# Kernel optimization log

Hardware: AMD Instinct MI355X
Metric: run time of the kernel (lower is better)

Reference implementation:

```python
import jax, jax.numpy as jnp
import numpy as np

B, T, C, NH, L, V = 2, 1024, 768, 12, 4, 50304
HS = C // NH  # 64


def _norm(x):
    # torch: (x - x.mean(-1)) / x.std(-1) with unbiased std (ddof=1)
    mu = jnp.mean(x, axis=-1, keepdims=True)
    sd = jnp.std(x, axis=-1, ddof=1, keepdims=True)
    return (x - mu) / sd


def setup_inputs() -> dict:
    key = jax.random.key(0)
    ks = jax.random.split(key, 8)
    idx = jax.random.randint(ks[0], (B, T), 0, V)
    wte = jax.random.normal(ks[1], (V, C), jnp.float32) * 0.02
    wpe = jax.random.normal(ks[2], (1024, C), jnp.float32) * 0.02
    c_attn_w = jax.random.normal(ks[3], (L, 3 * C, C), jnp.float32) * 0.02
    c_proj_w = jax.random.normal(ks[4], (L, C, C), jnp.float32) * 0.02
    w_decay = jax.random.uniform(ks[5], (L, C), jnp.float32)          # decay in [0,1)
    eta = jax.random.uniform(ks[6], (L, C), jnp.float32) * 0.01       # small, like 1/block_size init
    lm_head_w = jax.random.normal(ks[7], (V, C), jnp.float32) * 0.02
    return dict(idx=idx, wte=wte, wpe=wpe, c_attn_w=c_attn_w, c_proj_w=c_proj_w,
                w_decay=w_decay, eta=eta, lm_head_w=lm_head_w)


def _rwkv7_block(x, Wqkv, Wproj, wd, et):
    Bx, Tx, Cx = x.shape
    qkv = (x @ Wqkv.T).reshape(Bx, Tx, 3, NH, HS)
    qkv = _norm(qkv)
    # [T, B, nh, hs] each
    q = jnp.transpose(qkv[:, :, 0], (1, 0, 2, 3))
    k = jnp.transpose(qkv[:, :, 1], (1, 0, 2, 3))
    v = jnp.transpose(qkv[:, :, 2], (1, 0, 2, 3))
    q = jax.lax.erf(q)
    k = jax.lax.erf(k)
    wv = wd.reshape(NH, HS)   # decay per (head, channel i)
    ev = et.reshape(NH, HS)
    a = -k
    b = k * ev
    k_ = k * ev
    v_ = v

    def step(state, inp):
        q_t, a_t, b_t, k_t, v_t = inp
        # state: [B, nh, hs(i), hs(k)]
        sab = jnp.einsum('bhik,bhk,bhj->bhij', state, a_t, b_t)
        state = state * wv[None, :, :, None] + sab + jnp.einsum('bhj,bhi->bhij', k_t, v_t)
        out = jnp.einsum('bhj,bhij->bhi', q_t, state)
        return state, out

    state0 = jnp.zeros((Bx, NH, HS, HS), x.dtype)
    _, vt = jax.lax.scan(step, state0, (q, a, b, k_, v_))  # vt: [T, B, nh, hs]
    y = jnp.transpose(vt, (1, 0, 2, 3)).reshape(Bx, Tx, Cx) @ Wproj.T
    return x + y


def reference(idx, wte, wpe, c_attn_w, c_proj_w, w_decay, eta, lm_head_w):
    t = idx.shape[1]
    x = wte[idx] + wpe[:t][None]
    for l in range(L):
        x = _rwkv7_block(x, c_attn_w[l], c_proj_w[l], w_decay[l], eta[l])
    x = _norm(x)
    # targets=None path: logits for last position only
    logits = x[:, -1:, :] @ lm_head_w.T  # [B, 1, V]
    return logits
```

## Files before the change

kernel.cpp:

```cpp
#include <hip/hip_runtime.h>
#include <hip/hip_bf16.h>
#include <cmath>

using bf16   = __bf16;
using bf16x8 = __attribute__((ext_vector_type(8))) __bf16;
using bf16x4 = __attribute__((ext_vector_type(4))) __bf16;
using f32x4  = __attribute__((ext_vector_type(4))) float;
using u32x4  = __attribute__((ext_vector_type(4))) unsigned int;

__global__ __launch_bounds__(256) void cast4_kernel(const float* __restrict__ src,
                                                    bf16* __restrict__ dst, int n4) {
  int i = blockIdx.x * 256 + threadIdx.x;
  int stride = gridDim.x * 256;
  for (; i < n4; i += stride) {
    f32x4 v = ((const f32x4*)src)[i];
    bf16x4 o;
    o[0] = (bf16)v[0]; o[1] = (bf16)v[1]; o[2] = (bf16)v[2]; o[3] = (bf16)v[3];
    ((bf16x4*)dst)[i] = o;
  }
}

__global__ __launch_bounds__(256) void emb_kernel(const int* __restrict__ idx,
                                                  const float* __restrict__ wte,
                                                  const float* __restrict__ wpe,
                                                  float* __restrict__ xf,
                                                  bf16* __restrict__ xb) {
  int bt = blockIdx.x;
  int t = bt & 1023;
  int tok = idx[bt];
  const float* wr = wte + (long)tok * 768;
  const float* pr = wpe + (long)t * 768;
  for (int c = threadIdx.x; c < 768; c += 256) {
    float v = wr[c] + pr[c];
    xf[(long)bt * 768 + c] = v;
    xb[(long)bt * 768 + c] = (bf16)v;
  }
}

template <int PROJ>
__global__ __launch_bounds__(256) void gemm_kernel(const bf16* __restrict__ A,
                                                   const bf16* __restrict__ W,
                                                   float* __restrict__ out,
                                                   float* __restrict__ xf,
                                                   bf16* __restrict__ xb,
                                                   int N, int K) {
  __shared__ char ldsA[128 * 128];
  __shared__ char ldsB[128 * 128];
  const int tid = threadIdx.x;
  const int l = tid & 63, wid = tid >> 6;
  const int lr = l & 15, g = l >> 4;
  const int m0 = blockIdx.y * 128, n0 = blockIdx.x * 128;
  const int wm = wid >> 1, wn = wid & 1;

  f32x4 acc[4][4];
#pragma unroll
  for (int i = 0; i < 4; ++i)
#pragma unroll
    for (int j = 0; j < 4; ++j) acc[i][j] = {0.f, 0.f, 0.f, 0.f};

  for (int k0 = 0; k0 < K; k0 += 32) {
    __syncthreads();
#pragma unroll
    for (int it = 0; it < 2; ++it) {
      int slot = tid + it * 256;
      int row = slot >> 2, q = slot & 3;
      u32x4 da = *(const u32x4*)(A + (long)(m0 + row) * K + k0 + q * 8);
      *(u32x4*)(ldsA + row * 128 + ((q * 16) ^ ((row & 7) << 4))) = da;
      u32x4 db = *(const u32x4*)(W + (long)(n0 + row) * K + k0 + q * 8);
      *(u32x4*)(ldsB + row * 128 + ((q * 16) ^ ((row & 7) << 4))) = db;
    }
    __syncthreads();
    bf16x8 af[4], bfr[4];
#pragma unroll
    for (int it = 0; it < 4; ++it) {
      int row = wm * 64 + it * 16 + lr;
      af[it] = *(const bf16x8*)(ldsA + row * 128 + ((16 * g) ^ ((row & 7) << 4)));
    }
#pragma unroll
    for (int jt = 0; jt < 4; ++jt) {
      int row = wn * 64 + jt * 16 + lr;
      bfr[jt] = *(const bf16x8*)(ldsB + row * 128 + ((16 * g) ^ ((row & 7) << 4)));
    }
#pragma unroll
    for (int it = 0; it < 4; ++it)
#pragma unroll
      for (int jt = 0; jt < 4; ++jt)
        acc[it][jt] = __builtin_amdgcn_mfma_f32_16x16x32_bf16(af[it], bfr[jt], acc[it][jt], 0, 0, 0);
  }

#pragma unroll
  for (int it = 0; it < 4; ++it) {
#pragma unroll
    for (int jt = 0; jt < 4; ++jt) {
      int col = n0 + wn * 64 + jt * 16 + lr;
#pragma unroll
      for (int r = 0; r < 4; ++r) {
        int row = m0 + wm * 64 + it * 16 + g * 4 + r;
        if constexpr (PROJ) {
          long o = (long)row * 768 + col;
          float v = acc[it][jt][r] + xf[o];
          xf[o] = v;
          xb[o] = (bf16)v;
        } else {
          out[(long)row * N + col] = acc[it][jt][r];
        }
      }
    }
  }
}

__global__ __launch_bounds__(256) void normerf_kernel(const float* __restrict__ qkv,
                                                      const float* __restrict__ eta_l,
                                                      bf16* __restrict__ qG,
                                                      bf16* __restrict__ aG,
                                                      bf16* __restrict__ bG,
                                                      float* __restrict__ vG) {
  int gidx = blockIdx.x * 4 + (threadIdx.x >> 6);
  int lane = threadIdx.x & 63;
  int h = gidx % 12;
  int rest = gidx / 12;
  int s = rest % 3;
  int bt = rest / 3;
  float x = qkv[(long)bt * 2304 + s * 768 + h * 64 + lane];
  float mu = x;
#pragma unroll
  for (int o = 32; o; o >>= 1) mu += __shfl_xor(mu, o);
  mu *= (1.f / 64.f);
  float d = x - mu;
  float v2 = d * d;
#pragma unroll
  for (int o = 32; o; o >>= 1) v2 += __shfl_xor(v2, o);
  float sd = sqrtf(v2 * (1.f / 63.f));
  float gn = d / sd;
  int b = bt >> 10, t = bt & 1023;
  long base = ((long)(b * 12 + h) * 1024 + t) * 64 + lane;
  if (s == 0) {
    qG[base] = (bf16)erff(gn);
  } else if (s == 1) {
    float kh = erff(gn);
    aG[base] = (bf16)(-kh);
    bG[base] = (bf16)(kh * eta_l[h * 64 + lane]);
  } else {
    vG[base] = gn;
  }
}

__global__ __launch_bounds__(256) void gram_kernel(const bf16* __restrict__ aG,
                                                   const bf16* __restrict__ bG,
                                                   const bf16* __restrict__ qG,
                                                   float* __restrict__ GaG,
                                                   bf16* __restrict__ GqG,
                                                   bf16* __restrict__ bTG) {
  const int bh = blockIdx.x >> 6, ch = blockIdx.x & 63;
  __shared__ float as[16][68], bs[16][68], qs[16][68];
  const long tb = ((long)bh * 1024 + ch * 16) * 64;
  for (int i = threadIdx.x; i < 1024; i += 256) {
    int t = i >> 6, d = i & 63;
    as[t][d] = (float)aG[tb + i];
    bs[t][d] = (float)bG[tb + i];
    qs[t][d] = (float)qG[tb + i];
  }
  __syncthreads();
  const int t = threadIdx.x & 15, u = threadIdx.x >> 4;
  float dba = 0.f, dbq = 0.f;
#pragma unroll 4
  for (int d = 0; d < 64; ++d) {
    float bv = bs[u][d];
    dba += bv * as[t][d];
    dbq += bv * qs[t][d];
  }
  long g2 = (long)bh * 64 + ch;
  GaG[g2 * 256 + u * 16 + t] = (u < t) ? dba : 0.f;
  GqG[g2 * 512 + t * 32 + u] = (u <= t) ? (bf16)dbq : (bf16)0.f;
  GqG[g2 * 512 + t * 32 + 16 + u] = (bf16)0.f;
  int j = threadIdx.x >> 2, uq = threadIdx.x & 3;
  bf16x8 pkv;
#pragma unroll
  for (int uu = 0; uu < 8; ++uu) pkv[uu] = (uq < 2) ? (bf16)bs[uq * 8 + uu][j] : (bf16)0.f;
  *(bf16x8*)(bTG + g2 * 2048 + j * 32 + uq * 8) = pkv;
}

__global__ __launch_bounds__(256) void scan_kernel(const float* __restrict__ wdl,
                                                   const bf16* __restrict__ aG,
                                                   const bf16* __restrict__ qG,
                                                   const float* __restrict__ vG,
                                                   const float* __restrict__ GaG,
                                                   const bf16* __restrict__ GqG,
                                                   const bf16* __restrict__ bTG,
                                                   bf16* __restrict__ yG) {
  const int bh = blockIdx.x;
  const int b = bh / 12, h = bh - b * 12;
  const int tid = threadIdx.x;
  const int l = tid & 63, wid = tid >> 6;
  const int lr = l & 15, g = l >> 4;

  __shared__ char sA[2][16 * 128];
  __shared__ char sQ[2][16 * 128];
  __shared__ char sB[2][64 * 128];
  __shared__ char sG[2][16 * 128];
  __shared__ float sGa[2][16][16];
  __shared__ float sV[2][16][68];
  __shared__ char sS[64 * 128];
  __shared__ float sM[16][68];

  const float* wrow = wdl + h * 64;
  const int irow = wid * 16 + lr;
  const float w_rec = fmaxf(wrow[irow], 0.004f);
  const float winv_rec = 1.0f / w_rec;

  float wc[4], w15c[4], l2wc[4];
#pragma unroll
  for (int r = 0; r < 4; ++r) {
    int row = wid * 16 + g * 4 + r;
    float w = fmaxf(wrow[row], 0.004f);
    wc[r] = w;
    l2wc[r] = log2f(w);
    w15c[r] = exp2f(15.0f * l2wc[r]);
  }

  f32x4 Sf[4];
#pragma unroll
  for (int j = 0; j < 4; ++j) Sf[j] = {0.f, 0.f, 0.f, 0.f};

  const long hTD = (long)bh * 1024 * 64;

  u32x4 rAQ, rB, rGG;
  f32x4 rV;

  auto LOAD = [&](int c) {
    const long tb = hTD + (long)c * 16 * 64;
    const long g2 = (long)bh * 64 + c;
    if (tid < 128) {
      rAQ = *(const u32x4*)(aG + tb + (tid >> 3) * 64 + (tid & 7) * 8);
    } else {
      rAQ = *(const u32x4*)(qG + tb + ((tid - 128) >> 3) * 64 + ((tid - 128) & 7) * 8);
    }
    rB = *(const u32x4*)(bTG + g2 * 2048 + (tid >> 2) * 32 + (tid & 3) * 8);
    if (tid < 64) {
      rGG = *(const u32x4*)(GqG + g2 * 512 + (tid >> 2) * 32 + (tid & 3) * 8);
    } else if (tid < 128) {
      rGG = *(const u32x4*)(GaG + g2 * 256 + ((tid - 64) >> 2) * 16 + ((tid - 64) & 3) * 4);
    }
    rV = *(const f32x4*)(vG + tb + (tid >> 4) * 64 + (tid & 15) * 4);
  };

  auto STORE = [&](int nb) {
    if (tid < 128) {
      int t = tid >> 3, q = tid & 7;
      *(u32x4*)(sA[nb] + t * 128 + ((q * 16) ^ ((t & 7) << 4))) = rAQ;
    } else {
      int t = (tid - 128) >> 3, q = (tid - 128) & 7;
      *(u32x4*)(sQ[nb] + t * 128 + ((q * 16) ^ ((t & 7) << 4))) = rAQ;
    }
    {
      int j = tid >> 2, q = tid & 3;
      *(u32x4*)(sB[nb] + j * 128 + ((q * 16) ^ ((j & 7) << 4))) = rB;
    }
    if (tid < 64) {
      int t = tid >> 2, q = tid & 3;
      *(u32x4*)(sG[nb] + t * 128 + ((q * 16) ^ ((t & 7) << 4))) = rGG;
    } else if (tid < 128) {
      int u = (tid - 64) >> 2, q = (tid - 64) & 3;
      *(u32x4*)(&sGa[nb][u][q * 4]) = rGG;
    }
    {
      int t = tid >> 4, i4 = tid & 15;
      *(f32x4*)(&sV[nb][t][i4 * 4]) = rV;
    }
  };

  LOAD(0);
  STORE(0);
#pragma unroll
  for (int jt = 0; jt < 4; ++jt) {
#pragma unroll
    for (int r = 0; r < 4; ++r) {
      int row = wid * 16 + g * 4 + r;
      int d = jt * 16 + lr;
      *(bf16*)(sS + row * 128 + ((d * 2) ^ ((row & 7) << 4))) = (bf16)0.0f;
    }
  }
  __syncthreads();

  for (int ch = 0; ch < 64; ++ch) {
    const int cur = ch & 1, nxt = cur ^ 1;
    if (ch < 63) LOAD(ch + 1);

    f32x4 mf = {0.f, 0.f, 0.f, 0.f}, mqf = {0.f, 0.f, 0.f, 0.f};
#pragma unroll
    for (int s = 0; s < 2; ++s) {
      bf16x8 af = *(const bf16x8*)(sS + irow * 128 + ((64 * s + 16 * g) ^ ((irow & 7) << 4)));
      bf16x8 ba = *(const bf16x8*)(sA[cur] + lr * 128 + ((64 * s + 16 * g) ^ ((lr & 7) << 4)));
      bf16x8 bq = *(const bf16x8*)(sQ[cur] + lr * 128 + ((64 * s + 16 * g) ^ ((lr & 7) << 4)));
      mf = __builtin_amdgcn_mfma_f32_16x16x32_bf16(af, ba, mf, 0, 0, 0);
      mqf = __builtin_amdgcn_mfma_f32_16x16x32_bf16(af, bq, mqf, 0, 0, 0);
    }
#pragma unroll
    for (int r = 0; r < 4; ++r) sM[lr][wid * 16 + g * 4 + r] = mf[r];
    asm volatile("s_waitcnt lgkmcnt(0)" ::: "memory");
    __builtin_amdgcn_sched_barrier(0);

    float accr[16];
#pragma unroll
    for (int t = 0; t < 16; ++t) accr[t] = 0.f;
    bf16x8 zfrag;
#pragma unroll
    for (int i = 0; i < 8; ++i) zfrag[i] = (bf16)0.0f;
    float wp = 1.f, wpm1 = 0.f, wiv = 1.f;
#pragma unroll
    for (int u = 0; u < 16; ++u) {
      float mu = sM[u][irow];
      float vu = sV[cur][u][irow];
      float c = wp * mu + wpm1 * accr[u];
      float zt = wiv * (c + vu);
      zfrag[u & 7] = (g == (u >> 3)) ? (bf16)zt : zfrag[u & 7];
      f32x4 ga0 = *(const f32x4*)(&sGa[cur][u][0]);
      f32x4 ga1 = *(const f32x4*)(&sGa[cur][u][4]);
      f32x4 ga2 = *(const f32x4*)(&sGa[cur][u][8]);
      f32x4 ga3 = *(const f32x4*)(&sGa[cur][u][12]);
#pragma unroll
      for (int t = 0; t < 4; ++t) {
        accr[t] += ga0[t] * zt;
        accr[4 + t] += ga1[t] * zt;
        accr[8 + t] += ga2[t] * zt;
        accr[12 + t] += ga3[t] * zt;
      }
      wpm1 = wp;
      wp *= w_rec;
      wiv *= winv_rec;
    }

    {
      bf16x8 gq = *(const bf16x8*)(sG[cur] + lr * 128 + ((16 * g) ^ ((lr & 7) << 4)));
      f32x4 cy;
#pragma unroll
      for (int r = 0; r < 4; ++r) cy[r] = mqf[r] * wc[r];
      f32x4 yp = __builtin_amdgcn_mfma_f32_16x16x32_bf16(zfrag, gq, cy, 0, 0, 0);
      int t = lr;
      bf16x4 yo;
#pragma unroll
      for (int r = 0; r < 4; ++r) yo[r] = (bf16)(yp[r] * exp2f((float)t * l2wc[r]));
      long yoff = ((long)b * 1024 + ch * 16 + t) * 768 + h * 64 + wid * 16 + g * 4;
      *(bf16x4*)(yG + yoff) = yo;
    }

#pragma unroll
    for (int jt = 0; jt < 4; ++jt) {
      int jrow = jt * 16 + lr;
      bf16x8 bb = *(const bf16x8*)(sB[cur] + jrow * 128 + ((16 * g) ^ ((jrow & 7) << 4)));
      f32x4 cs;
#pragma unroll
      for (int r = 0; r < 4; ++r) cs[r] = Sf[jt][r] * wc[r];
      f32x4 ns = __builtin_amdgcn_mfma_f32_16x16x32_bf16(zfrag, bb, cs, 0, 0, 0);
#pragma unroll
      for (int r = 0; r < 4; ++r) Sf[jt][r] = ns[r] * w15c[r];
    }

#pragma unroll
    for (int jt = 0; jt < 4; ++jt) {
#pragma unroll
      for (int r = 0; r < 4; ++r) {
        int row = wid * 16 + g * 4 + r;
        int d = jt * 16 + lr;
        *(bf16*)(sS + row * 128 + ((d * 2) ^ ((row & 7) << 4))) = (bf16)Sf[jt][r];
      }
    }

    if (ch < 63) STORE(nxt);
    __syncthreads();
  }
}

__global__ __launch_bounds__(256) void finalnorm_kernel(const float* __restrict__ xf,
                                                        float* __restrict__ xn) {
  __shared__ float red[4];
  int tid = threadIdx.x;
  for (int b = 0; b < 2; ++b) {
    const float* xr = xf + ((long)b * 1024 + 1023) * 768;
    float s = 0.f;
    for (int c = tid; c < 768; c += 256) s += xr[c];
#pragma unroll
    for (int o = 32; o; o >>= 1) s += __shfl_xor(s, o);
    if ((tid & 63) == 0) red[tid >> 6] = s;
    __syncthreads();
    float mu = (red[0] + red[1] + red[2] + red[3]) * (1.f / 768.f);
    __syncthreads();
    float s2 = 0.f;
    for (int c = tid; c < 768; c += 256) {
      float d = xr[c] - mu;
      s2 += d * d;
    }
#pragma unroll
    for (int o = 32; o; o >>= 1) s2 += __shfl_xor(s2, o);
    if ((tid & 63) == 0) red[tid >> 6] = s2;
    __syncthreads();
    float sd = sqrtf((red[0] + red[1] + red[2] + red[3]) * (1.f / 767.f));
    for (int c = tid; c < 768; c += 256) xn[b * 768 + c] = (xr[c] - mu) / sd;
    __syncthreads();
  }
}

__global__ __launch_bounds__(256) void lmhead_kernel(const float* __restrict__ W,
                                                     const float* __restrict__ xn,
                                                     float* __restrict__ out) {
  int l = threadIdx.x & 63, wid = threadIdx.x >> 6;
  int v0 = blockIdx.x * 64 + wid * 16;
  f32x4 x0[3], x1[3];
#pragma unroll
  for (int i = 0; i < 3; ++i) {
    x0[i] = *(const f32x4*)(xn + l * 4 + i * 256);
    x1[i] = *(const f32x4*)(xn + 768 + l * 4 + i * 256);
  }
  for (int vi = 0; vi < 16; ++vi) {
    const float* wr = W + (long)(v0 + vi) * 768;
    float pa = 0.f, pb = 0.f;
#pragma unroll
    for (int i = 0; i < 3; ++i) {
      f32x4 wv = *(const f32x4*)(wr + l * 4 + i * 256);
#pragma unroll
      for (int r = 0; r < 4; ++r) {
        pa += wv[r] * x0[i][r];
        pb += wv[r] * x1[i][r];
      }
    }
#pragma unroll
    for (int o = 32; o; o >>= 1) {
      pa += __shfl_xor(pa, o);
      pb += __shfl_xor(pb, o);
    }
    if (l == 0) {
      out[v0 + vi] = pa;
      out[50304 + v0 + vi] = pb;
    }
  }
}

extern "C" void kernel_launch(void* const* d_in, const int* in_sizes, int n_in,
                              void* d_out, int out_size, void* d_ws, size_t ws_size,
                              hipStream_t stream) {
  (void)in_sizes; (void)n_in; (void)out_size; (void)ws_size;
  const int*   idx      = (const int*)d_in[0];
  const float* wte      = (const float*)d_in[1];
  const float* wpe      = (const float*)d_in[2];
  const float* c_attn_w = (const float*)d_in[3];
  const float* c_proj_w = (const float*)d_in[4];
  const float* w_decay  = (const float*)d_in[5];
  const float* eta      = (const float*)d_in[6];
  const float* lm_head  = (const float*)d_in[7];
  float* out = (float*)d_out;

  char* ws = (char*)d_ws;
  size_t off = 0;
  auto alloc = [&](size_t bytes) -> char* {
    char* p = ws + off;
    off = (off + bytes + 255) & ~(size_t)255;
    return p;
  };
  float* xf   = (float*)alloc(2L * 1024 * 768 * 4);
  bf16*  xb   = (bf16*)alloc(2L * 1024 * 768 * 2);
  float* qkv  = (float*)alloc(2L * 1024 * 2304 * 4);
  bf16*  qGp  = (bf16*)alloc(24L * 1024 * 64 * 2);
  bf16*  aGp  = (bf16*)alloc(24L * 1024 * 64 * 2);
  bf16*  bGp  = (bf16*)alloc(24L * 1024 * 64 * 2);
  float* vGp  = (float*)alloc(24L * 1024 * 64 * 4);
  float* GaGp = (float*)alloc(24L * 64 * 256 * 4);
  bf16*  GqGp = (bf16*)alloc(24L * 64 * 512 * 2);
  bf16*  bTGp = (bf16*)alloc(24L * 64 * 2048 * 2);
  bf16*  yGp  = (bf16*)alloc(2L * 1024 * 768 * 2);
  bf16*  WqB  = (bf16*)alloc(4L * 2304 * 768 * 2);
  bf16*  WpB  = (bf16*)alloc(4L * 768 * 768 * 2);
  float* xn   = (float*)alloc(2L * 768 * 4);

  cast4_kernel<<<dim3(2048), dim3(256), 0, stream>>>(c_attn_w, WqB, 4 * 2304 * 768 / 4);
  cast4_kernel<<<dim3(1024), dim3(256), 0, stream>>>(c_proj_w, WpB, 4 * 768 * 768 / 4);
  emb_kernel<<<dim3(2048), dim3(256), 0, stream>>>(idx, wte, wpe, xf, xb);

  for (int l = 0; l < 4; ++l) {
    gemm_kernel<0><<<dim3(18, 16), dim3(256), 0, stream>>>(
        xb, WqB + (long)l * 2304 * 768, qkv, nullptr, nullptr, 2304, 768);
    normerf_kernel<<<dim3(18432), dim3(256), 0, stream>>>(
        qkv, eta + l * 768, qGp, aGp, bGp, vGp);
    gram_kernel<<<dim3(1536), dim3(256), 0, stream>>>(aGp, bGp, qGp, GaGp, GqGp, bTGp);
    scan_kernel<<<dim3(24), dim3(256), 0, stream>>>(
        w_decay + l * 768, aGp, qGp, vGp, GaGp, GqGp, bTGp, yGp);
    gemm_kernel<1><<<dim3(6, 16), dim3(256), 0, stream>>>(
        yGp, WpB + (long)l * 768 * 768, nullptr, xf, xb, 768, 768);
  }

  finalnorm_kernel<<<dim3(1), dim3(256), 0, stream>>>(xf, xn);
  lmhead_kernel<<<dim3(786), dim3(256), 0, stream>>>(lm_head, xn, out);
}
```

Before: 822.0 us.

## Fuse norm/erf into gram kernel and double-chunk scan prefetch

Merges the per-head normalization/erf kernel into the chunk gram kernel, so each block loads its raw qkv tile once and builds the gram products from shared memory without a global round trip for the b tensor. The scan kernel now prefetches two chunks per pipeline stage, which halves the number of block-wide barriers. It also tightens the shared-memory layout of the B and Gq tiles to 64-byte rows and gathers the per-chunk work into a COMPUTE lambda. The cost is more registers and shared memory in the scan, which runs only 24 blocks and is latency bound.

Result: faster. 797.9 us (-2.9%).

```diff
diff --git a/kernel.cpp b/kernel.cpp
--- a/kernel.cpp
+++ b/kernel.cpp
@@ -109,59 +109,65 @@
   }
 }
 
-__global__ __launch_bounds__(256) void normerf_kernel(const float* __restrict__ qkv,
-                                                      const float* __restrict__ eta_l,
-                                                      bf16* __restrict__ qG,
-                                                      bf16* __restrict__ aG,
-                                                      bf16* __restrict__ bG,
-                                                      float* __restrict__ vG) {
-  int gidx = blockIdx.x * 4 + (threadIdx.x >> 6);
-  int lane = threadIdx.x & 63;
-  int h = gidx % 12;
-  int rest = gidx / 12;
-  int s = rest % 3;
-  int bt = rest / 3;
-  float x = qkv[(long)bt * 2304 + s * 768 + h * 64 + lane];
-  float mu = x;
-#pragma unroll
-  for (int o = 32; o; o >>= 1) mu += __shfl_xor(mu, o);
-  mu *= (1.f / 64.f);
-  float d = x - mu;
-  float v2 = d * d;
-#pragma unroll
-  for (int o = 32; o; o >>= 1) v2 += __shfl_xor(v2, o);
-  float sd = sqrtf(v2 * (1.f / 63.f));
-  float gn = d / sd;
-  int b = bt >> 10, t = bt & 1023;
-  long base = ((long)(b * 12 + h) * 1024 + t) * 64 + lane;
-  if (s == 0) {
-    qG[base] = (bf16)erff(gn);
-  } else if (s == 1) {
-    float kh = erff(gn);
-    aG[base] = (bf16)(-kh);
-    bG[base] = (bf16)(kh * eta_l[h * 64 + lane]);
-  } else {
-    vG[base] = gn;
-  }
-}
-
-__global__ __launch_bounds__(256) void gram_kernel(const bf16* __restrict__ aG,
-                                                   const bf16* __restrict__ bG,
-                                                   const bf16* __restrict__ qG,
-                                                   float* __restrict__ GaG,
-                                                   bf16* __restrict__ GqG,
-                                                   bf16* __restrict__ bTG) {
+__global__ __launch_bounds__(256) void normgram_kernel(const float* __restrict__ qkv,
+                                                       const float* __restrict__ eta_l,
+                                                       bf16* __restrict__ qG,
+                                                       bf16* __restrict__ aG,
+                                                       float* __restrict__ vG,
+                                                       float* __restrict__ GaG,
+                                                       bf16* __restrict__ GqG,
+                                                       bf16* __restrict__ bTG) {
   const int bh = blockIdx.x >> 6, ch = blockIdx.x & 63;
+  const int b = bh / 12, h = bh - b * 12;
+  const int tid = threadIdx.x;
+  __shared__ float raw[48][68];
   __shared__ float as[16][68], bs[16][68], qs[16][68];
-  const long tb = ((long)bh * 1024 + ch * 16) * 64;
-  for (int i = threadIdx.x; i < 1024; i += 256) {
-    int t = i >> 6, d = i & 63;
-    as[t][d] = (float)aG[tb + i];
-    bs[t][d] = (float)bG[tb + i];
-    qs[t][d] = (float)qG[tb + i];
+
+  const long qbase = ((long)(b * 1024 + ch * 16)) * 2304 + h * 64;
+#pragma unroll
+  for (int i = 0; i < 3; ++i) {
+    int slot = tid + i * 256;
+    int c4 = slot & 15, sgrp = slot >> 4;
+    int t = sgrp / 3, s = sgrp - 3 * t;
+    f32x4 d = *(const f32x4*)(qkv + qbase + (long)t * 2304 + s * 768 + c4 * 4);
+    *(f32x4*)(&raw[sgrp][c4 * 4]) = d;
   }
   __syncthreads();
-  const int t = threadIdx.x & 15, u = threadIdx.x >> 4;
+
+  const int l = tid & 63, w = tid >> 6;
+  const float ev = eta_l[h * 64 + l];
+#pragma unroll
+  for (int j = 0; j < 12; ++j) {
+    int sgrp = w * 12 + j;
+    int t = sgrp / 3, s = sgrp - 3 * t;
+    float x = raw[sgrp][l];
+    float mu = x;
+#pragma unroll
+    for (int o = 32; o; o >>= 1) mu += __shfl_xor(mu, o);
+    mu *= (1.f / 64.f);
+    float d = x - mu;
+    float v2 = d * d;
+#pragma unroll
+    for (int o = 32; o; o >>= 1) v2 += __shfl_xor(v2, o);
+    float sd = sqrtf(v2 * (1.f / 63.f));
+    float gn = d / sd;
+    long base = ((long)bh * 1024 + ch * 16 + t) * 64 + l;
+    if (s == 0) {
+      float qv = erff(gn);
+      qs[t][l] = qv;
+      qG[base] = (bf16)qv;
+    } else if (s == 1) {
+      float kh = erff(gn);
+      as[t][l] = -kh;
+      bs[t][l] = kh * ev;
+      aG[base] = (bf16)(-kh);
+    } else {
+      vG[base] = gn;
+    }
+  }
+  __syncthreads();
+
+  const int t = tid & 15, u = tid >> 4;
   float dba = 0.f, dbq = 0.f;
 #pragma unroll 4
   for (int d = 0; d < 64; ++d) {
@@ -173,11 +179,11 @@
   GaG[g2 * 256 + u * 16 + t] = (u < t) ? dba : 0.f;
   GqG[g2 * 512 + t * 32 + u] = (u <= t) ? (bf16)dbq : (bf16)0.f;
   GqG[g2 * 512 + t * 32 + 16 + u] = (bf16)0.f;
-  int j = threadIdx.x >> 2, uq = threadIdx.x & 3;
+  int jj = tid >> 2, uq = tid & 3;
   bf16x8 pkv;
 #pragma unroll
-  for (int uu = 0; uu < 8; ++uu) pkv[uu] = (uq < 2) ? (bf16)bs[uq * 8 + uu][j] : (bf16)0.f;
-  *(bf16x8*)(bTG + g2 * 2048 + j * 32 + uq * 8) = pkv;
+  for (int uu = 0; uu < 8; ++uu) pkv[uu] = (uq < 2) ? (bf16)bs[uq * 8 + uu][jj] : (bf16)0.f;
+  *(bf16x8*)(bTG + g2 * 2048 + jj * 32 + uq * 8) = pkv;
 }
 
 __global__ __launch_bounds__(256) void scan_kernel(const float* __restrict__ wdl,
@@ -194,12 +200,12 @@
   const int l = tid & 63, wid = tid >> 6;
   const int lr = l & 15, g = l >> 4;
 
-  __shared__ char sA[2][16 * 128];
-  __shared__ char sQ[2][16 * 128];
-  __shared__ char sB[2][64 * 128];
-  __shared__ char sG[2][16 * 128];
-  __shared__ float sGa[2][16][16];
-  __shared__ float sV[2][16][68];
+  __shared__ char sA[2][2][16 * 128];
+  __shared__ char sQ[2][2][16 * 128];
+  __shared__ char sB[2][2][64 * 64];
+  __shared__ char sG[2][2][16 * 64];
+  __shared__ float sGa[2][2][16][16];
+  __shared__ float sV[2][2][16][64];
   __shared__ char sS[64 * 128];
   __shared__ float sM[16][68];
 
@@ -224,53 +230,147 @@
 
   const long hTD = (long)bh * 1024 * 64;
 
-  u32x4 rAQ, rB, rGG;
-  f32x4 rV;
-
-  auto LOAD = [&](int c) {
-    const long tb = hTD + (long)c * 16 * 64;
-    const long g2 = (long)bh * 64 + c;
-    if (tid < 128) {
-      rAQ = *(const u32x4*)(aG + tb + (tid >> 3) * 64 + (tid & 7) * 8);
-    } else {
-      rAQ = *(const u32x4*)(qG + tb + ((tid - 128) >> 3) * 64 + ((tid - 128) & 7) * 8);
-    }
-    rB = *(const u32x4*)(bTG + g2 * 2048 + (tid >> 2) * 32 + (tid & 3) * 8);
-    if (tid < 64) {
-      rGG = *(const u32x4*)(GqG + g2 * 512 + (tid >> 2) * 32 + (tid & 3) * 8);
-    } else if (tid < 128) {
-      rGG = *(const u32x4*)(GaG + g2 * 256 + ((tid - 64) >> 2) * 16 + ((tid - 64) & 3) * 4);
-    }
-    rV = *(const f32x4*)(vG + tb + (tid >> 4) * 64 + (tid & 15) * 4);
+  u32x4 rAQ[2], rB[2], rGG[2];
+  f32x4 rV[2];
+
+  auto LOAD2 = [&](int c0) {
+#pragma unroll
+    for (int k = 0; k < 2; ++k) {
+      const int c = c0 + k;
+      const long tb = hTD + (long)c * 16 * 64;
+      const long g2 = (long)bh * 64 + c;
+      if (tid < 128) {
+        rAQ[k] = *(const u32x4*)(aG + tb + (tid >> 3) * 64 + (tid & 7) * 8);
+      } else {
+        rAQ[k] = *(const u32x4*)(qG + tb + ((tid - 128) >> 3) * 64 + ((tid - 128) & 7) * 8);
+      }
+      rB[k] = *(const u32x4*)(bTG + g2 * 2048 + (tid >> 2) * 32 + (tid & 3) * 8);
+      if (tid < 64) {
+        rGG[k] = *(const u32x4*)(GqG + g2 * 512 + (tid >> 2) * 32 + (tid & 3) * 8);
+      } else if (tid < 128) {
+        rGG[k] = *(const u32x4*)(GaG + g2 * 256 + ((tid - 64) >> 2) * 16 + ((tid - 64) & 3) * 4);
+      }
+      rV[k] = *(const f32x4*)(vG + tb + (tid >> 4) * 64 + (tid & 15) * 4);
+    }
   };
 
-  auto STORE = [&](int nb) {
-    if (tid < 128) {
-      int t = tid >> 3, q = tid & 7;
-      *(u32x4*)(sA[nb] + t * 128 + ((q * 16) ^ ((t & 7) << 4))) = rAQ;
-    } else {
-      int t = (tid - 128) >> 3, q = (tid - 128) & 7;
-      *(u32x4*)(sQ[nb] + t * 128 + ((q * 16) ^ ((t & 7) << 4))) = rAQ;
-    }
+  auto STORE2 = [&](int nb) {
+#pragma unroll
+    for (int k = 0; k < 2; ++k) {
+      if (tid < 128) {
+        int t = tid >> 3, q = tid & 7;
+        *(u32x4*)(sA[nb][k] + t * 128 + ((q * 16) ^ ((t & 7) << 4))) = rAQ[k];
+      } else {
+        int t = (tid - 128) >> 3, q = (tid - 128) & 7;
+        *(u32x4*)(sQ[nb][k] + t * 128 + ((q * 16) ^ ((t & 7) << 4))) = rAQ[k];
+      }
+      {
+        int j = tid >> 2, q = tid & 3;
+        *(u32x4*)(sB[nb][k] + j * 64 + ((q * 16) ^ ((j & 3) << 4))) = rB[k];
+      }
+      if (tid < 64) {
+        int t = tid >> 2, q = tid & 3;
+        *(u32x4*)(sG[nb][k] + t * 64 + ((q * 16) ^ ((t & 3) << 4))) = rGG[k];
+      } else if (tid < 128) {
+        int u = (tid - 64) >> 2, q = (tid - 64) & 3;
+        *(u32x4*)(&sGa[nb][k][u][q * 4]) = rGG[k];
+      }
+      {
+        int t = tid >> 4, i4 = tid & 15;
+        *(f32x4*)(&sV[nb][k][t][i4 * 4]) = rV[k];
+      }
+    }
+  };
+
+  auto COMPUTE = [&](int cur, int cip, int ch) {
+    const char* pA = sA[cur][cip];
+    const char* pQ = sQ[cur][cip];
+    const char* pB = sB[cur][cip];
+    const char* pG = sG[cur][cip];
+    const float* pGa = &sGa[cur][cip][0][0];
+    const float* pV = &sV[cur][cip][0][0] + irow;
+    const float* pM = &sM[0][0] + irow;
+
+    asm volatile("s_waitcnt lgkmcnt(0)" ::: "memory");
+    __builtin_amdgcn_sched_barrier(0);
+
+    f32x4 mf = {0.f, 0.f, 0.f, 0.f}, mqf = {0.f, 0.f, 0.f, 0.f};
+#pragma unroll
+    for (int s = 0; s < 2; ++s) {
+      bf16x8 af = *(const bf16x8*)(sS + irow * 128 + ((64 * s + 16 * g) ^ ((irow & 7) << 4)));
+      bf16x8 ba = *(const bf16x8*)(pA + lr * 128 + ((64 * s + 16 * g) ^ ((lr & 7) << 4)));
+      bf16x8 bq = *(const bf16x8*)(pQ + lr * 128 + ((64 * s + 16 * g) ^ ((lr & 7) << 4)));
+      mf = __builtin_amdgcn_mfma_f32_16x16x32_bf16(af, ba, mf, 0, 0, 0);
+      mqf = __builtin_amdgcn_mfma_f32_16x16x32_bf16(af, bq, mqf, 0, 0, 0);
+    }
+#pragma unroll
+    for (int r = 0; r < 4; ++r) sM[lr][wid * 16 + g * 4 + r] = mf[r];
+    asm volatile("s_waitcnt lgkmcnt(0)" ::: "memory");
+    __builtin_amdgcn_sched_barrier(0);
+
+    f32x4 acc4[4];
+#pragma unroll
+    for (int t = 0; t < 4; ++t) acc4[t] = {0.f, 0.f, 0.f, 0.f};
+    bf16x8 zfrag;
+#pragma unroll
+    for (int i = 0; i < 8; ++i) zfrag[i] = (bf16)0.0f;
+    float wp = 1.f, wpm1 = 0.f, wiv = 1.f;
+#pragma unroll
+    for (int u = 0; u < 16; ++u) {
+      float muv = pM[u * 68];
+      float vu = pV[u * 64];
+      float c = wp * muv + wpm1 * acc4[u >> 2][u & 3];
+      float zt = wiv * (c + vu);
+      zfrag[u & 7] = (g == (u >> 3)) ? (bf16)zt : zfrag[u & 7];
+      f32x4 ztv = {zt, zt, zt, zt};
+#pragma unroll
+      for (int q = 0; q < 4; ++q) {
+        f32x4 ga = *(const f32x4*)(pGa + u * 16 + q * 4);
+        acc4[q] = __builtin_elementwise_fma(ga, ztv, acc4[q]);
+      }
+      wpm1 = wp;
+      wp *= w_rec;
+      wiv *= winv_rec;
+    }
+
+#pragma unroll
+    for (int jt = 0; jt < 4; ++jt) {
+      int jrow = jt * 16 + lr;
+      bf16x8 bb = *(const bf16x8*)(pB + jrow * 64 + ((16 * g) ^ ((jrow & 3) << 4)));
+      f32x4 cs;
+#pragma unroll
+      for (int r = 0; r < 4; ++r) cs[r] = Sf[jt][r] * wc[r];
+      f32x4 ns = __builtin_amdgcn_mfma_f32_16x16x32_bf16(zfrag, bb, cs, 0, 0, 0);
+#pragma unroll
+      for (int r = 0; r < 4; ++r) Sf[jt][r] = ns[r] * w15c[r];
+    }
+
+#pragma unroll
+    for (int jt = 0; jt < 4; ++jt) {
+#pragma unroll
+      for (int r = 0; r < 4; ++r) {
+        int row = wid * 16 + g * 4 + r;
+        int d = jt * 16 + lr;
+        *(bf16*)(sS + row * 128 + ((d * 2) ^ ((row & 7) << 4))) = (bf16)Sf[jt][r];
+      }
+    }
+
     {
-      int j = tid >> 2, q = tid & 3;
-      *(u32x4*)(sB[nb] + j * 128 + ((q * 16) ^ ((j & 7) << 4))) = rB;
-    }
-    if (tid < 64) {
-      int t = tid >> 2, q = tid & 3;
-      *(u32x4*)(sG[nb] + t * 128 + ((q * 16) ^ ((t & 7) << 4))) = rGG;
-    } else if (tid < 128) {
-      int u = (tid - 64) >> 2, q = (tid - 64) & 3;
-      *(u32x4*)(&sGa[nb][u][q * 4]) = rGG;
-    }
-    {
-      int t = tid >> 4, i4 = tid & 15;
-      *(f32x4*)(&sV[nb][t][i4 * 4]) = rV;
+      bf16x8 gq = *(const bf16x8*)(pG + lr * 64 + ((16 * g) ^ ((lr & 3) << 4)));
+      f32x4 cy;
+#pragma unroll
+      for (int r = 0; r < 4; ++r) cy[r] = mqf[r] * wc[r];
+      f32x4 yp = __builtin_amdgcn_mfma_f32_16x16x32_bf16(zfrag, gq, cy, 0, 0, 0);
+      bf16x4 yo;
+#pragma unroll
+      for (int r = 0; r < 4; ++r) yo[r] = (bf16)(yp[r] * exp2f((float)lr * l2wc[r]));
+      long yoff = ((long)b * 1024 + ch * 16 + lr) * 768 + h * 64 + wid * 16 + g * 4;
+      *(bf16x4*)(yG + yoff) = yo;
     }
   };
 
-  LOAD(0);
-  STORE(0);
+  LOAD2(0);
+  STORE2(0);
 #pragma unroll
   for (int jt = 0; jt < 4; ++jt) {
 #pragma unroll
@@ -282,91 +382,12 @@
   }
   __syncthreads();
 
-  for (int ch = 0; ch < 64; ++ch) {
-    const int cur = ch & 1, nxt = cur ^ 1;
-    if (ch < 63) LOAD(ch + 1);
-
-    f32x4 mf = {0.f, 0.f, 0.f, 0.f}, mqf = {0.f, 0.f, 0.f, 0.f};
-#pragma unroll
-    for (int s = 0; s < 2; ++s) {
-      bf16x8 af = *(const bf16x8*)(sS + irow * 128 + ((64 * s + 16 * g) ^ ((irow & 7) << 4)));
-      bf16x8 ba = *(const bf16x8*)(sA[cur] + lr * 128 + ((64 * s + 16 * g) ^ ((lr & 7) << 4)));
-      bf16x8 bq = *(const bf16x8*)(sQ[cur] + lr * 128 + ((64 * s + 16 * g) ^ ((lr & 7) << 4)));
-      mf = __builtin_amdgcn_mfma_f32_16x16x32_bf16(af, ba, mf, 0, 0, 0);
-      mqf = __builtin_amdgcn_mfma_f32_16x16x32_bf16(af, bq, mqf, 0, 0, 0);
-    }
-#pragma unroll
-    for (int r = 0; r < 4; ++r) sM[lr][wid * 16 + g * 4 + r] = mf[r];
-    asm volatile("s_waitcnt lgkmcnt(0)" ::: "memory");
-    __builtin_amdgcn_sched_barrier(0);
-
-    float accr[16];
-#pragma unroll
-    for (int t = 0; t < 16; ++t) accr[t] = 0.f;
-    bf16x8 zfrag;
-#pragma unroll
-    for (int i = 0; i < 8; ++i) zfrag[i] = (bf16)0.0f;
-    float wp = 1.f, wpm1 = 0.f, wiv = 1.f;
-#pragma unroll
-    for (int u = 0; u < 16; ++u) {
-      float mu = sM[u][irow];
-      float vu = sV[cur][u][irow];
-      float c = wp * mu + wpm1 * accr[u];
-      float zt = wiv * (c + vu);
-      zfrag[u & 7] = (g == (u >> 3)) ? (bf16)zt : zfrag[u & 7];
-      f32x4 ga0 = *(const f32x4*)(&sGa[cur][u][0]);
-      f32x4 ga1 = *(const f32x4*)(&sGa[cur][u][4]);
-      f32x4 ga2 = *(const f32x4*)(&sGa[cur][u][8]);
-      f32x4 ga3 = *(const f32x4*)(&sGa[cur][u][12]);
-#pragma unroll
-      for (int t = 0; t < 4; ++t) {
-        accr[t] += ga0[t] * zt;
-        accr[4 + t] += ga1[t] * zt;
-        accr[8 + t] += ga2[t] * zt;
-        accr[12 + t] += ga3[t] * zt;
-      }
-      wpm1 = wp;
-      wp *= w_rec;
-      wiv *= winv_rec;
-    }
-
-    {
-      bf16x8 gq = *(const bf16x8*)(sG[cur] + lr * 128 + ((16 * g) ^ ((lr & 7) << 4)));
-      f32x4 cy;
-#pragma unroll
-      for (int r = 0; r < 4; ++r) cy[r] = mqf[r] * wc[r];
-      f32x4 yp = __builtin_amdgcn_mfma_f32_16x16x32_bf16(zfrag, gq, cy, 0, 0, 0);
-      int t = lr;
-      bf16x4 yo;
-#pragma unroll
-      for (int r = 0; r < 4; ++r) yo[r] = (bf16)(yp[r] * exp2f((float)t * l2wc[r]));
-      long yoff = ((long)b * 1024 + ch * 16 + t) * 768 + h * 64 + wid * 16 + g * 4;
-      *(bf16x4*)(yG + yoff) = yo;
-    }
-
-#pragma unroll
-    for (int jt = 0; jt < 4; ++jt) {
-      int jrow = jt * 16 + lr;
-      bf16x8 bb = *(const bf16x8*)(sB[cur] + jrow * 128 + ((16 * g) ^ ((jrow & 7) << 4)));
-      f32x4 cs;
-#pragma unroll
-      for (int r = 0; r < 4; ++r) cs[r] = Sf[jt][r] * wc[r];
-      f32x4 ns = __builtin_amdgcn_mfma_f32_16x16x32_bf16(zfrag, bb, cs, 0, 0, 0);
-#pragma unroll
-      for (int r = 0; r < 4; ++r) Sf[jt][r] = ns[r] * w15c[r];
-    }
-
-#pragma unroll
-    for (int jt = 0; jt < 4; ++jt) {
-#pragma unroll
-      for (int r = 0; r < 4; ++r) {
-        int row = wid * 16 + g * 4 + r;
-        int d = jt * 16 + lr;
-        *(bf16*)(sS + row * 128 + ((d * 2) ^ ((row & 7) << 4))) = (bf16)Sf[jt][r];
-      }
-    }
-
-    if (ch < 63) STORE(nxt);
+  for (int gp = 0; gp < 32; ++gp) {
+    const int cur = gp & 1;
+    if (gp < 31) LOAD2(2 * gp + 2);
+    COMPUTE(cur, 0, 2 * gp);
+    COMPUTE(cur, 1, 2 * gp + 1);
+    if (gp < 31) STORE2(cur ^ 1);
     __syncthreads();
   }
 }
@@ -461,7 +482,6 @@
   float* qkv  = (float*)alloc(2L * 1024 * 2304 * 4);
   bf16*  qGp  = (bf16*)alloc(24L * 1024 * 64 * 2);
   bf16*  aGp  = (bf16*)alloc(24L * 1024 * 64 * 2);
-  bf16*  bGp  = (bf16*)alloc(24L * 1024 * 64 * 2);
   float* vGp  = (float*)alloc(24L * 1024 * 64 * 4);
   float* GaGp = (float*)alloc(24L * 64 * 256 * 4);
   bf16*  GqGp = (bf16*)alloc(24L * 64 * 512 * 2);
@@ -478,9 +498,8 @@
   for (int l = 0; l < 4; ++l) {
     gemm_kernel<0><<<dim3(18, 16), dim3(256), 0, stream>>>(
         xb, WqB + (long)l * 2304 * 768, qkv, nullptr, nullptr, 2304, 768);
-    normerf_kernel<<<dim3(18432), dim3(256), 0, stream>>>(
-        qkv, eta + l * 768, qGp, aGp, bGp, vGp);
-    gram_kernel<<<dim3(1536), dim3(256), 0, stream>>>(aGp, bGp, qGp, GaGp, GqGp, bTGp);
+    normgram_kernel<<<dim3(1536), dim3(256), 0, stream>>>(
+        qkv, eta + l * 768, qGp, aGp, vGp, GaGp, GqGp, bTGp);
     scan_kernel<<<dim3(24), dim3(256), 0, stream>>>(
         w_decay + l * 768, aGp, qGp, vGp, GaGp, GqGp, bTGp, yGp);
     gemm_kernel<1><<<dim3(6, 16), dim3(256), 0, stream>>>(
```
